# Performance work log

Measured on AMD Instinct MI355X. Metric: run time of the kernel, lower is better.

## Reference

```python
import jax, jax.numpy as jnp
import numpy as np
from jax import lax

BN_EPS = 1e-5
ARC_EPS = 1e-7
M = 0.5   # margin
S = 64.0  # scale


def _conv_block(x, w, g, b, a, stride):
    # Conv2d(bias=False, VALID) + BatchNorm2d (training mode, batch stats) + PReLU
    y = lax.conv_general_dilated(x, w, (stride, stride), 'VALID',
                                 dimension_numbers=('NCHW', 'OIHW', 'NCHW'))
    mu = y.mean((0, 2, 3), keepdims=True)
    var = ((y - mu) ** 2).mean((0, 2, 3), keepdims=True)
    y = (y - mu) * lax.rsqrt(var + BN_EPS) * g.reshape(1, -1, 1, 1) + b.reshape(1, -1, 1, 1)
    return jnp.where(y > 0, y, a * y)


def setup_inputs() -> dict:
    key = jax.random.key(0)
    ks = jax.random.split(key, 16)
    N = 4096
    d = {}
    d['x'] = jax.random.normal(ks[0], (N, 1, 28, 28), jnp.float32)
    d['labels'] = jax.random.randint(ks[1], (N,), 0, 10)
    conv_shapes = [(32, 1, 1, 1), (64, 32, 3, 3), (32, 64, 1, 1),
                   (64, 32, 3, 3), (32, 64, 1, 1), (64, 32, 3, 3)]
    for i, s in enumerate(conv_shapes):
        fan_in = s[1] * s[2] * s[3]
        d[f'cw{i}'] = jax.random.normal(ks[2 + i], s, jnp.float32) / np.sqrt(fan_in)
        d[f'bg{i}'] = jnp.ones((s[0],), jnp.float32)
        d[f'bb{i}'] = jnp.zeros((s[0],), jnp.float32)
        d[f'pa{i}'] = jnp.full((), 0.25, jnp.float32)  # nn.PReLU() single param
    d['lw1'] = jax.random.normal(ks[8], (128, 1024), jnp.float32) * (1.0 / np.sqrt(1024))
    d['lg1'] = jnp.ones((128,), jnp.float32)
    d['lb1'] = jnp.zeros((128,), jnp.float32)
    d['pl1'] = jnp.full((), 0.25, jnp.float32)
    d['lw2'] = jax.random.normal(ks[9], (2, 128), jnp.float32) * (1.0 / np.sqrt(128))
    d['lb2'] = jnp.zeros((2,), jnp.float32)
    d['aw'] = jax.random.normal(ks[10], (10, 2), jnp.float32) * 0.2  # ArcLoss fc weight (out, in)
    return d


def reference(x, labels, cw0, cw1, cw2, cw3, cw4, cw5,
              bg0, bb0, bg1, bb1, bg2, bb2, bg3, bb3, bg4, bb4, bg5, bb5,
              pa0, pa1, pa2, pa3, pa4, pa5,
              lw1, lg1, lb1, pl1, lw2, lb2, aw):
    strides = (1, 2, 1, 2, 1, 1)
    ws = (cw0, cw1, cw2, cw3, cw4, cw5)
    gs = (bg0, bg1, bg2, bg3, bg4, bg5)
    bs = (bb0, bb1, bb2, bb3, bb4, bb5)
    pas = (pa0, pa1, pa2, pa3, pa4, pa5)
    h = x
    for w, g, b, a, st in zip(ws, gs, bs, pas, strides):
        h = _conv_block(h, w, g, b, a, st)  # final: (N, 64, 4, 4)
    flat = h.reshape(h.shape[0], -1)        # (N, 1024)
    z = flat @ lw1.T                         # (N, 128)
    mu = z.mean(0)
    var = ((z - mu) ** 2).mean(0)
    z = (z - mu) * lax.rsqrt(var + BN_EPS) * lg1 + lb1
    z = jnp.where(z > 0, z, pl1 * z)
    features = z @ lw2.T + lb2               # (N, 2)

    # ArcLoss. NOTE: original torch code's weight-normalization loop is a no-op
    # (rebinds local var), so fc weight is used UN-normalized; only x is normalized.
    xn = features / jnp.linalg.norm(features, axis=-1, keepdims=True)
    wf = xn @ aw.T                           # (N, 10) logits
    n = wf.shape[0]
    tgt = wf[jnp.arange(n), labels]          # vectorized diag gather
    num = S * jnp.cos(jnp.arccos(jnp.clip(tgt, -1.0 + ARC_EPS, 1.0 - ARC_EPS)) + M)
    # vectorized exclusion sum: sum_j exp(s*wf[i,j]) minus the target column
    den = jnp.exp(num) + jnp.sum(jnp.exp(S * wf), axis=1) - jnp.exp(S * tgt)
    loss = -jnp.mean(num - jnp.log(den))
    return (features, wf, loss)
```

## Files before the change

kernel.cpp:

```cpp
#include <hip/hip_runtime.h>
#include <hip/hip_bf16.h>
#include <math.h>


typedef __attribute__((ext_vector_type(8))) short s16x8;
typedef __attribute__((ext_vector_type(16))) float f32x16;

__device__ __forceinline__ unsigned short f2bf(float f) {
  __hip_bfloat16 h = __float2bfloat16(f);
  unsigned short u;
  __builtin_memcpy(&u, &h, 2);
  return u;
}
__device__ __forceinline__ float bf2f(unsigned short h) {
  union { unsigned int u; float f; } t; t.u = ((unsigned int)h) << 16; return t.f;
}

__global__ __launch_bounds__(256) void kRedX(const float* __restrict__ x,
                                             float* __restrict__ part) {
  int tid = threadIdx.x;
  int b = blockIdx.x;
  const float4* x4 = (const float4*)x;
  float s = 0.f, q = 0.f;
  for (size_t i = (size_t)b * 256 + tid; i < 802816; i += (size_t)512 * 256) {
    float4 v = x4[i];
    s += v.x + v.y + v.z + v.w;
    q += v.x * v.x + v.y * v.y + v.z * v.z + v.w * v.w;
  }
#pragma unroll
  for (int off = 32; off; off >>= 1) {
    s += __shfl_down(s, off);
    q += __shfl_down(q, off);
  }
  __shared__ float ls[4][2];
  int w = tid >> 6;
  if ((tid & 63) == 0) { ls[w][0] = s; ls[w][1] = q; }
  __syncthreads();
  if (tid == 0) {
    part[b * 2]     = ls[0][0] + ls[1][0] + ls[2][0] + ls[3][0];
    part[b * 2 + 1] = ls[0][1] + ls[1][1] + ls[2][1] + ls[3][1];
  }
}

__global__ __launch_bounds__(256) void kRedPart(const float* __restrict__ part,
                                                float* __restrict__ outp, int nb, int C2) {
  int slot = blockIdx.x;
  int tid = threadIdx.x;
  float s = 0.f;
  for (int i = tid; i < nb; i += 256) s += part[(size_t)i * C2 + slot];
#pragma unroll
  for (int off = 32; off; off >>= 1) s += __shfl_down(s, off);
  __shared__ float ls[4];
  if ((tid & 63) == 0) ls[tid >> 6] = s;
  __syncthreads();
  if (tid == 0) outp[slot] = ls[0] + ls[1] + ls[2] + ls[3];
}

__global__ __launch_bounds__(256) void kPrepW(const float* __restrict__ cw1,
                                              unsigned short* __restrict__ wf) {
  int tid = threadIdx.x;
  int lane = tid & 63, fb = tid >> 6;
  int m = lane & 31, kg = lane >> 5;
  for (int pass = 0; pass < 9; pass++) {
    int f = pass * 4 + fb;
    int tap = f >> 2, rem = f & 3, kt = rem >> 1, nt = rem & 1;
    int o = nt * 32 + m;
    int kb = kt * 16 + kg * 8;
    union { s16x8 v; unsigned short e[8]; } u;
#pragma unroll
    for (int j = 0; j < 8; j++)
      u.e[j] = f2bf(cw1[(size_t)o * 288 + (size_t)(kb + j) * 9 + tap]);
    ((s16x8*)wf)[f * 64 + lane] = u.v;
  }
}

__global__ __launch_bounds__(256) void kPrepW3(const float* __restrict__ cw3,
                                               unsigned short* __restrict__ wf3) {
  int tid = threadIdx.x;
  int lane = tid & 63, fq = tid >> 6;
  int m = lane & 31, kg = lane >> 5;
  for (int pass = 0; pass < 9; pass++) {
    int f = pass * 4 + fq;
    int s = f >> 1, nt = f & 1;
    int tap = s >> 1;
    int o = nt * 32 + m;
    int c0 = (s & 1) * 16 + kg * 8;
    union { s16x8 v; unsigned short e[8]; } u;
#pragma unroll
    for (int j = 0; j < 8; j++)
      u.e[j] = f2bf(cw3[(size_t)o * 288 + (size_t)(c0 + j) * 9 + tap]);
    ((s16x8*)wf3)[f * 64 + lane] = u.v;
  }
}

__global__ __launch_bounds__(256) void kPrepW1x1(const float* __restrict__ wgt,
                                                 unsigned short* __restrict__ wfb) {
  int tid = threadIdx.x;
  int l = tid & 63, ks = tid >> 6;
  int o = l & 31, kg = l >> 5;
  union { s16x8 v; unsigned short e[8]; } u;
#pragma unroll
  for (int j = 0; j < 8; j++) {
    int c = ks * 16 + kg * 8 + j;
    u.e[j] = f2bf(wgt[o * 64 + c]);
  }
  ((s16x8*)wfb)[ks * 64 + l] = u.v;
}

__global__ __launch_bounds__(256, 2) void kConv1(
    const float* __restrict__ x, const float* __restrict__ cw0,
    const float* __restrict__ bg0, const float* __restrict__ bb0,
    const float* __restrict__ pa0, const unsigned short* __restrict__ wf,
    const float* __restrict__ sx, unsigned short* __restrict__ y1b,
    float* __restrict__ part) {
  __shared__ __align__(16) unsigned short h0t[25088];
  __shared__ __align__(16) float xbuf[784];
  __shared__ float s0[32], t0[32];
  int tid = threadIdx.x;
  int n = blockIdx.x;
  int l = tid & 63, w = tid >> 6;
  int nt = w & 1, mh = w >> 1;
  int m = l & 31, kg = l >> 5;

  s16x8 bfr[9][2];
  const s16x8* wfp = (const s16x8*)wf;
#pragma unroll
  for (int tap = 0; tap < 9; tap++)
#pragma unroll
    for (int kt = 0; kt < 2; kt++)
      bfr[tap][kt] = wfp[(tap * 4 + kt * 2 + nt) * 64 + l];

  if (tid < 196) ((float4*)xbuf)[tid] = ((const float4*)(x + (size_t)n * 784))[tid];
  if (tid < 32) {
    const float invM = 1.0f / (4096.0f * 784.0f);
    float mux = sx[0] * invM;
    float varx = fmaxf(sx[1] * invM - mux * mux, 0.0f);
    float w0 = cw0[tid];
    float inv = rsqrtf(w0 * w0 * varx + 1e-5f);
    float sc = w0 * bg0[tid] * inv;
    s0[tid] = sc;
    t0[tid] = bb0[tid] - mux * sc;
  }
  __syncthreads();

  float a0p = *pa0;
  int g = tid & 3;
  float sg[8], tg[8];
#pragma unroll
  for (int j = 0; j < 8; j++) { sg[j] = s0[g * 8 + j]; tg[j] = t0[g * 8 + j]; }
  char* h0b = (char*)h0t;
  int koffW = g * 16;
  for (int t = 0; t < 13; t++) {
    int p = (tid >> 2) + t * 64;
    if (p < 784) {
      float xv = xbuf[p];
      union { s16x8 v; unsigned short e[8]; } u;
#pragma unroll
      for (int j = 0; j < 8; j++) {
        float v = fmaf(xv, sg[j], tg[j]);
        v = v > 0.f ? v : a0p * v;
        u.e[j] = f2bf(v);
      }
      int ad = ((p << 6) + koffW) ^ (((p >> 1) & 7) << 4);
      *(s16x8*)(h0b + ad) = u.v;
    }
  }
  __syncthreads();

  int pixb[3];
#pragma unroll
  for (int mt = 0; mt < 3; mt++) {
    int p = (mh * 3 + mt) * 32 + m;
    p = p > 168 ? 168 : p;
    pixb[mt] = (p / 13) * 56 + (p % 13) * 2;
  }
  int koffA = kg * 16;

#define Z16 {0.f,0.f,0.f,0.f, 0.f,0.f,0.f,0.f, 0.f,0.f,0.f,0.f, 0.f,0.f,0.f,0.f}
  f32x16 acc0 = Z16, acc1 = Z16, acc2 = Z16;

#define MT_STEP(ACC, MTL) { int pb = pixb[MTL]; \
  _Pragma("unroll") for (int tap = 0; tap < 9; tap++) { \
    int pix = pb + (tap / 3) * 28 + (tap % 3); \
    int ad = ((pix << 6) + koffA) ^ (((pix >> 1) & 7) << 4); \
    s16x8 a0 = *(const s16x8*)(h0b + ad); \
    s16x8 a1 = *(const s16x8*)(h0b + (ad ^ 32)); \
    ACC = __builtin_amdgcn_mfma_f32_32x32x16_bf16(a0, bfr[tap][0], ACC, 0, 0, 0); \
    ACC = __builtin_amdgcn_mfma_f32_32x32x16_bf16(a1, bfr[tap][1], ACC, 0, 0, 0); \
  } }

  MT_STEP(acc0, 0)
  MT_STEP(acc1, 1)
  MT_STEP(acc2, 2)
#undef MT_STEP

  __syncthreads();
  unsigned short* ystage = h0t;
  float* sSf = xbuf;
  float* sQf = xbuf + 128;
  float s = 0.f, q = 0.f;
  int och = nt * 32 + m;
#define ST_MT(ACC, MTL) { int pbase = (mh * 3 + MTL) * 32 + (kg << 2); \
  _Pragma("unroll") for (int r = 0; r < 16; r++) { \
    int p = pbase + (r & 3) + ((r >> 2) << 3); \
    if (p < 169) { float v = ACC[r]; \
      ystage[p * 64 + och] = f2bf(v); s += v; q += v * v; } } }

  ST_MT(acc0, 0)
  ST_MT(acc1, 1)
  ST_MT(acc2, 2)
#undef ST_MT

  s += __shfl_xor(s, 32);
  q += __shfl_xor(q, 32);
  if (l < 32) { sSf[w * 32 + l] = s; sQf[w * 32 + l] = q; }
  __syncthreads();
  {
    const s16x8* src8 = (const s16x8*)ystage;
    s16x8* dst8 = (s16x8*)(y1b + (size_t)n * 10816);
    for (int e = tid; e < 1352; e += 256) dst8[e] = src8[e];
  }
  if (tid < 64) {
    int o = tid, wv = o >> 5;
    part[(size_t)n * 128 + o] = sSf[wv * 32 + (o & 31)] + sSf[(wv + 2) * 32 + (o & 31)];
  } else if (tid < 128) {
    int o = tid - 64, wv = o >> 5;
    part[(size_t)n * 128 + 64 + o] = sQf[wv * 32 + (o & 31)] + sQf[(wv + 2) * 32 + (o & 31)];
  }
}

__global__ __launch_bounds__(256, 4) void kConv1x1m(
    const unsigned short* __restrict__ wfb, const float* __restrict__ g,
    const float* __restrict__ b, const float* __restrict__ pa,
    const float* __restrict__ stats, float invM,
    const unsigned short* __restrict__ in, unsigned short* __restrict__ outb,
    float* __restrict__ part) {
  __shared__ __align__(16) unsigned short hs[128 * 64];
  __shared__ float scs[64], shs[64];
  __shared__ float sS[4][32], sQ[4][32];
  int tid = threadIdx.x;
  size_t r0 = (size_t)blockIdx.x * 128;
  int l = tid & 63, w = tid >> 6;
  int m = l & 31, kg = l >> 5;

  s16x8 bfr[4];
  const s16x8* bp = (const s16x8*)wfb;
#pragma unroll
  for (int ks = 0; ks < 4; ks++) bfr[ks] = bp[ks * 64 + l];

  if (tid < 64) {
    float mu = stats[tid] * invM;
    float va = fmaxf(stats[64 + tid] * invM - mu * mu, 0.0f);
    float iv = rsqrtf(va + 1e-5f);
    float sc = g[tid] * iv;
    scs[tid] = sc;
    shs[tid] = b[tid] - mu * sc;
  }
  __syncthreads();
  float al = *pa;
  char* hb = (char*)hs;
#pragma unroll
  for (int i = 0; i < 4; i++) {
    int e = tid + i * 256;
    int row = e >> 3, seg = e & 7;
    union { s16x8 v; unsigned short e8[8]; } u, o8;
    u.v = *(const s16x8*)(in + (r0 + row) * 64 + seg * 8);
#pragma unroll
    for (int j = 0; j < 8; j++) {
      int c = seg * 8 + j;
      float h = fmaf(bf2f(u.e8[j]), scs[c], shs[c]);
      h = h > 0.f ? h : al * h;
      o8.e8[j] = f2bf(h);
    }
    int ad = (row * 128 + seg * 16) ^ ((row & 7) << 4);
    *(s16x8*)(hb + ad) = o8.v;
  }
  __syncthreads();

#define Z16 {0.f,0.f,0.f,0.f, 0.f,0.f,0.f,0.f, 0.f,0.f,0.f,0.f, 0.f,0.f,0.f,0.f}
  f32x16 acc = Z16;
#undef Z16
  int rloc = w * 32 + m;
  int abase = (rloc * 128 + kg * 16) ^ ((rloc & 7) << 4);
#pragma unroll
  for (int ks = 0; ks < 4; ks++) {
    s16x8 a = *(const s16x8*)(hb + (abase ^ (ks * 32)));
    acc = __builtin_amdgcn_mfma_f32_32x32x16_bf16(a, bfr[ks], acc, 0, 0, 0);
  }

  float ss = 0.f, qq = 0.f;
#pragma unroll
  for (int rr = 0; rr < 16; rr++) {
    int rowt = (rr & 3) + ((rr >> 2) << 3) + (kg << 2);
    float v = acc[rr];
    outb[(r0 + (size_t)w * 32 + rowt) * 32 + m] = f2bf(v);
    ss += v; qq += v * v;
  }
  ss += __shfl_xor(ss, 32);
  qq += __shfl_xor(qq, 32);
  if (l < 32) { sS[w][l] = ss; sQ[w][l] = qq; }
  __syncthreads();
  if (tid < 32) {
    part[(size_t)blockIdx.x * 64 + tid] = sS[0][tid] + sS[1][tid] + sS[2][tid] + sS[3][tid];
  } else if (tid < 64) {
    int o = tid - 32;
    part[(size_t)blockIdx.x * 64 + 32 + o] = sQ[0][o] + sQ[1][o] + sQ[2][o] + sQ[3][o];
  }
}

__global__ __launch_bounds__(256, 3) void kConv3m(
    const unsigned short* __restrict__ wf3, const float* __restrict__ g,
    const float* __restrict__ b, const float* __restrict__ pa,
    const float* __restrict__ stats, const unsigned short* __restrict__ in,
    unsigned short* __restrict__ outb, float* __restrict__ part) {
  __shared__ __align__(16) unsigned short h2t[169 * 32];
  __shared__ float scs[32], shs[32];
  __shared__ float sS[4][32], sQ[4][32];
  int tid = threadIdx.x;
  int n = blockIdx.x;
  int l = tid & 63, w = tid >> 6;
  int nt = w & 1, mt = w >> 1;
  int m = l & 31, kg = l >> 5;

  s16x8 bfr[18];
  const s16x8* wfp = (const s16x8*)wf3;
#pragma unroll
  for (int s = 0; s < 18; s++) bfr[s] = wfp[(s * 2 + nt) * 64 + l];

  if (tid < 32) {
    const float invM = 1.0f / 692224.0f;
    float mu = stats[tid] * invM;
    float va = fmaxf(stats[32 + tid] * invM - mu * mu, 0.0f);
    float iv = rsqrtf(va + 1e-5f);
    float sc = g[tid] * iv;
    scs[tid] = sc;
    shs[tid] = b[tid] - mu * sc;
  }
  __syncthreads();
  float al = *pa;
  char* hb = (char*)h2t;
  for (int e = tid; e < 676; e += 256) {
    int p = e >> 2, q = e & 3;
    union { s16x8 v; unsigned short e8[8]; } u, o8;
    u.v = ((const s16x8*)(in + ((size_t)n * 169 + p) * 32))[q];
#pragma unroll
    for (int j = 0; j < 8; j++) {
      int c = q * 8 + j;
      float h = fmaf(bf2f(u.e8[j]), scs[c], shs[c]);
      h = h > 0.f ? h : al * h;
      o8.e8[j] = f2bf(h);
    }
    int ad = ((p << 6) + q * 16) ^ (((p >> 1) & 7) << 4);
    *(s16x8*)(hb + ad) = o8.v;
  }
  __syncthreads();

  int p = mt * 32 + m;
  p = p > 35 ? 35 : p;
  int pixb = (p / 6) * 26 + (p % 6) * 2;

#define Z16 {0.f,0.f,0.f,0.f, 0.f,0.f,0.f,0.f, 0.f,0.f,0.f,0.f, 0.f,0.f,0.f,0.f}
  f32x16 acc = Z16;
#undef Z16
#pragma unroll
  for (int s = 0; s < 18; s++) {
    int tap = s >> 1;
    int pix = pixb + (tap / 3) * 13 + (tap % 3);
    int ad = ((pix << 6) + (s & 1) * 32 + kg * 16) ^ (((pix >> 1) & 7) << 4);
    s16x8 a = *(const s16x8*)(hb + ad);
    acc = __builtin_amdgcn_mfma_f32_32x32x16_bf16(a, bfr[s], acc, 0, 0, 0);
  }

  float ss = 0.f, qq = 0.f;
  int och = nt * 32 + m;
#pragma unroll
  for (int r = 0; r < 16; r++) {
    int row = (r & 3) + ((r >> 2) << 3) + (kg << 2);
    int pp = mt * 32 + row;
    if (pp < 36) {
      float v = acc[r];
      outb[((size_t)n * 36 + pp) * 64 + och] = f2bf(v);
      ss += v; qq += v * v;
    }
  }
  ss += __shfl_xor(ss, 32);
  qq += __shfl_xor(qq, 32);
  if (l < 32) { sS[w][l] = ss; sQ[w][l] = qq; }
  __syncthreads();
  if (tid < 64) {
    int o = tid, wv = o >> 5;
    part[(size_t)n * 128 + o] = sS[wv][o & 31] + sS[wv + 2][o & 31];
  } else if (tid < 128) {
    int o = tid - 64, wv = o >> 5;
    part[(size_t)n * 128 + 64 + o] = sQ[wv][o & 31] + sQ[wv + 2][o & 31];
  }
}

__global__ __launch_bounds__(128) void kConv5m(
    const unsigned short* __restrict__ wf5, const float* __restrict__ g,
    const float* __restrict__ b, const float* __restrict__ pa,
    const float* __restrict__ stats, const unsigned short* __restrict__ in,
    float* __restrict__ outb, float* __restrict__ part) {
  __shared__ __align__(16) unsigned short h4t[2 * 1280];
  __shared__ float scs[32], shs[32];
  int tid = threadIdx.x;
  int nA = blockIdx.x * 2;
  int l = tid & 63, w = tid >> 6;
  int m = l & 31, kg = l >> 5;

  s16x8 bfr[18];
  const s16x8* wfp = (const s16x8*)wf5;
#pragma unroll
  for (int s = 0; s < 18; s++) bfr[s] = wfp[(s * 2 + w) * 64 + l];

  if (tid < 32) {
    const float invM = 1.0f / 147456.0f;
    float mu = stats[tid] * invM;
    float va = fmaxf(stats[32 + tid] * invM - mu * mu, 0.0f);
    float iv = rsqrtf(va + 1e-5f);
    float sc = g[tid] * iv;
    scs[tid] = sc;
    shs[tid] = b[tid] - mu * sc;
  }
  __syncthreads();
  float al = *pa;
  char* hb = (char*)h4t;
  for (int e = tid; e < 288; e += 128) {
    int img = e >= 144;
    int rem = e - img * 144;
    int p = rem >> 2, q = rem & 3;
    union { s16x8 v; unsigned short e8[8]; } u, o8;
    u.v = ((const s16x8*)(in + ((size_t)(nA + img) * 36 + p) * 32))[q];
#pragma unroll
    for (int j = 0; j < 8; j++) {
      int c = q * 8 + j;
      float h = fmaf(bf2f(u.e8[j]), scs[c], shs[c]);
      h = h > 0.f ? h : al * h;
      o8.e8[j] = f2bf(h);
    }
    int ad = img * 2560 + (((p << 6) + q * 16) ^ (((p >> 1) & 7) << 4));
    *(s16x8*)(hb + ad) = o8.v;
  }
  __syncthreads();

  int imgl = m >> 4;
  int pl = m & 15;
  int pixb = (pl >> 2) * 6 + (pl & 3);
  int ibase = imgl * 2560;

#define Z16 {0.f,0.f,0.f,0.f, 0.f,0.f,0.f,0.f, 0.f,0.f,0.f,0.f, 0.f,0.f,0.f,0.f}
  f32x16 acc = Z16;
#undef Z16
#pragma unroll
  for (int s = 0; s < 18; s++) {
    int tap = s >> 1;
    int pix = pixb + (tap / 3) * 6 + (tap % 3);
    int ad = ibase + (((pix << 6) + (s & 1) * 32 + kg * 16) ^ (((pix >> 1) & 7) << 4));
    s16x8 a = *(const s16x8*)(hb + ad);
    acc = __builtin_amdgcn_mfma_f32_32x32x16_bf16(a, bfr[s], acc, 0, 0, 0);
  }

  float ss = 0.f, qq = 0.f;
  int och = w * 32 + m;
#pragma unroll
  for (int r = 0; r < 16; r++) {
    int row = (r & 3) + ((r >> 2) << 3) + (kg << 2);
    int img = row >> 4, p = row & 15;
    float v = acc[r];
    outb[(size_t)(nA + img) * 1024 + och * 16 + p] = v;
    ss += v; qq += v * v;
  }
  ss += __shfl_xor(ss, 32);
  qq += __shfl_xor(qq, 32);
  if (l < 32) {
    part[(size_t)blockIdx.x * 128 + w * 32 + l] = ss;
    part[(size_t)blockIdx.x * 128 + 64 + w * 32 + l] = qq;
  }
}

__global__ __launch_bounds__(256) void kPrepLW(const float* __restrict__ lw1,
                                               unsigned short* __restrict__ wfl) {
  int tid = threadIdx.x;
  int lane = tid & 63, fq = tid >> 6;
  int m = lane & 31, kg = lane >> 5;
  for (int pp = 0; pp < 4; pp++) {
    int f_idx = (blockIdx.x * 4 + pp) * 4 + fq;
    int ks = f_idx >> 2, nt = f_idx & 3;
    int f = nt * 32 + m;
    int kb = ks * 16 + kg * 8;
    const float4* src = (const float4*)(lw1 + (size_t)f * 1024 + kb);
    float4 v0 = src[0], v1 = src[1];
    float t[8] = {v0.x, v0.y, v0.z, v0.w, v1.x, v1.y, v1.z, v1.w};
    union { s16x8 v; unsigned short e[8]; } u;
#pragma unroll
    for (int j = 0; j < 8; j++) u.e[j] = f2bf(t[j]);
    ((s16x8*)wfl)[f_idx * 64 + lane] = u.v;
  }
}

__global__ __launch_bounds__(128) void kFC1m(
    const unsigned short* __restrict__ wfl, const float* __restrict__ g,
    const float* __restrict__ b, const float* __restrict__ pa,
    const float* __restrict__ stats, const float* __restrict__ y5,
    float* __restrict__ z, float* __restrict__ part) {
  __shared__ __align__(16) unsigned short hs[32 * 1024];
  __shared__ float scs[64], shs[64];
  int tid = threadIdx.x;
  int n0 = blockIdx.x * 32;
  if (tid < 64) {
    const float invM = 1.0f / 65536.0f;
    float mu = stats[tid] * invM;
    float va = fmaxf(stats[64 + tid] * invM - mu * mu, 0.0f);
    float iv = rsqrtf(va + 1e-5f);
    float sc = g[tid] * iv;
    scs[tid] = sc;
    shs[tid] = b[tid] - mu * sc;
  }
  __syncthreads();
  float al = *pa;
  char* hb = (char*)hs;
  for (int i = 0; i < 32; i++) {
    int sgi = tid + i * 128;
    int nn = sgi >> 7, k8 = sgi & 127;
    int c = k8 >> 1;
    float sc = scs[c], sh = shs[c];
    const float4* src = (const float4*)(y5 + (size_t)(n0 + nn) * 1024 + k8 * 8);
    float4 v0 = src[0], v1 = src[1];
    float t[8] = {v0.x, v0.y, v0.z, v0.w, v1.x, v1.y, v1.z, v1.w};
    union { s16x8 v; unsigned short e[8]; } u;
#pragma unroll
    for (int j = 0; j < 8; j++) {
      float h = fmaf(t[j], sc, sh);
      h = h > 0.f ? h : al * h;
      u.e[j] = f2bf(h);
    }
    int ad = (nn * 2048 + k8 * 16) ^ ((nn & 7) << 4);
    *(s16x8*)(hb + ad) = u.v;
  }
  __syncthreads();

  int l = tid & 63, w = tid >> 6;
  int m = l & 31, kg = l >> 5;
#define Z16 {0.f,0.f,0.f,0.f, 0.f,0.f,0.f,0.f, 0.f,0.f,0.f,0.f, 0.f,0.f,0.f,0.f}
  f32x16 acc0 = Z16, acc1 = Z16;
#undef Z16
  const s16x8* bp = (const s16x8*)wfl;
  int abase = (m * 2048 + kg * 16) ^ ((m & 7) << 4);
#pragma unroll 4
  for (int ks = 0; ks < 64; ks++) {
    s16x8 a = *(const s16x8*)(hb + (abase ^ (ks * 32)));
    s16x8 b0 = bp[(ks * 4 + 2 * w + 0) * 64 + l];
    s16x8 b1 = bp[(ks * 4 + 2 * w + 1) * 64 + l];
    acc0 = __builtin_amdgcn_mfma_f32_32x32x16_bf16(a, b0, acc0, 0, 0, 0);
    acc1 = __builtin_amdgcn_mfma_f32_32x32x16_bf16(a, b1, acc1, 0, 0, 0);
  }

  float s0 = 0.f, q0 = 0.f, s1 = 0.f, q1 = 0.f;
  int f0c = (2 * w) * 32 + m, f1c = (2 * w + 1) * 32 + m;
#pragma unroll
  for (int r = 0; r < 16; r++) {
    int n = (r & 3) + ((r >> 2) << 3) + (kg << 2);
    float v0 = acc0[r], v1 = acc1[r];
    z[(size_t)(n0 + n) * 128 + f0c] = v0;
    z[(size_t)(n0 + n) * 128 + f1c] = v1;
    s0 += v0; q0 += v0 * v0; s1 += v1; q1 += v1 * v1;
  }
  s0 += __shfl_xor(s0, 32); q0 += __shfl_xor(q0, 32);
  s1 += __shfl_xor(s1, 32); q1 += __shfl_xor(q1, 32);
  if (l < 32) {
    size_t base = (size_t)blockIdx.x * 256;
    part[base + w * 64 + m] = s0;
    part[base + w * 64 + 32 + m] = s1;
    part[base + 128 + w * 64 + m] = q0;
    part[base + 128 + w * 64 + 32 + m] = q1;
  }
}

__global__ __launch_bounds__(256) void kFC2Arc(
    const float* __restrict__ z, const float* __restrict__ s6,
    const float* __restrict__ lg1, const float* __restrict__ lb1,
    const float* __restrict__ pl1, const float* __restrict__ lw2,
    const float* __restrict__ lb2, const float* __restrict__ aw,
    const int* __restrict__ labels, float* __restrict__ out,
    float* __restrict__ lpart) {
  __shared__ float scz[128], shz[128], w2a[128], w2b[128];
  __shared__ float awl[20];
  __shared__ float lred[4];
  int tid = threadIdx.x;
  if (tid < 128) {
    const float invM = 1.0f / 4096.0f;
    float mu = s6[tid] * invM;
    float va = fmaxf(s6[128 + tid] * invM - mu * mu, 0.0f);
    float iv = rsqrtf(va + 1e-5f);
    float sc = lg1[tid] * iv;
    scz[tid] = sc;
    shz[tid] = lb1[tid] - mu * sc;
    w2a[tid] = lw2[tid];
    w2b[tid] = lw2[128 + tid];
  }
  if (tid < 20) awl[tid] = aw[tid];
  __syncthreads();
  float al = *pl1;
  int n = blockIdx.x * 256 + tid;
  const float4* zr = (const float4*)(z + (size_t)n * 128);
  float f0 = lb2[0], f1 = lb2[1];
#pragma unroll
  for (int kb = 0; kb < 32; kb++) {
    float4 v = zr[kb];
    float hv[4] = {v.x, v.y, v.z, v.w};
#pragma unroll
    for (int u = 0; u < 4; u++) {
      int k = kb * 4 + u;
      float h = fmaf(hv[u], scz[k], shz[k]);
      h = h > 0.f ? h : al * h;
      f0 = fmaf(h, w2a[k], f0);
      f1 = fmaf(h, w2b[k], f1);
    }
  }
  out[(size_t)n * 2] = f0;
  out[(size_t)n * 2 + 1] = f1;
  float nrm = sqrtf(fmaxf(f0 * f0 + f1 * f1, 1e-30f));
  float xn0 = f0 / nrm, xn1 = f1 / nrm;
  int lab = labels[n];
  float wv[10];
  float m64 = -3.4e38f;
#pragma unroll
  for (int j = 0; j < 10; j++) {
    float w = xn0 * awl[2 * j] + xn1 * awl[2 * j + 1];
    wv[j] = w;
    out[8192 + (size_t)n * 10 + j] = w;
    m64 = fmaxf(m64, 64.0f * w);
  }
  float tgt = wv[0];
#pragma unroll
  for (int j = 1; j < 10; j++) if (j == lab) tgt = wv[j];
  if (lab == 0) tgt = wv[0];
  const float CLO = (float)(-1.0 + 1e-7);
  const float CHI = (float)(1.0 - 1e-7);
  float t = fminf(fmaxf(tgt, CLO), CHI);
  float num = 64.0f * (t * 0.87758256189037276f - 0.47942553860420301f * sqrtf(fmaxf(1.0f - t * t, 0.0f)));
  float L = fmaxf(num, m64);
  float dsum = expf(num - L) - expf(64.0f * tgt - L);
#pragma unroll
  for (int j = 0; j < 10; j++) dsum += expf(64.0f * wv[j] - L);
  dsum = fmaxf(dsum, 1e-30f);
  float li = num - (L + logf(dsum));
#pragma unroll
  for (int off = 32; off; off >>= 1) li += __shfl_down(li, off);
  if ((tid & 63) == 0) lred[tid >> 6] = li;
  __syncthreads();
  if (tid == 0) lpart[blockIdx.x] = lred[0] + lred[1] + lred[2] + lred[3];
}

__global__ void kFinal(const float* __restrict__ lpart, float* __restrict__ out) {
  int tid = threadIdx.x;
  float v = (tid < 16) ? lpart[tid] : 0.f;
#pragma unroll
  for (int off = 8; off; off >>= 1) v += __shfl_down(v, off);
  if (tid == 0) out[49152] = -v * (1.0f / 4096.0f);
}

extern "C" void kernel_launch(void* const* d_in, const int* in_sizes, int n_in,
                              void* d_out, int out_size, void* d_ws, size_t ws_size,
                              hipStream_t stream) {
  const float* x   = (const float*)d_in[0];
  const int* labels = (const int*)d_in[1];
  const float* cw0 = (const float*)d_in[2];
  const float* bg0 = (const float*)d_in[3];
  const float* bb0 = (const float*)d_in[4];
  const float* pa0 = (const float*)d_in[5];
  const float* cw1 = (const float*)d_in[6];
  const float* bg1 = (const float*)d_in[7];
  const float* bb1 = (const float*)d_in[8];
  const float* pa1 = (const float*)d_in[9];
  const float* cw2 = (const float*)d_in[10];
  const float* bg2 = (const float*)d_in[11];
  const float* bb2 = (const float*)d_in[12];
  const float* pa2 = (const float*)d_in[13];
  const float* cw3 = (const float*)d_in[14];
  const float* bg3 = (const float*)d_in[15];
  const float* bb3 = (const float*)d_in[16];
  const float* pa3 = (const float*)d_in[17];
  const float* cw4 = (const float*)d_in[18];
  const float* bg4 = (const float*)d_in[19];
  const float* bb4 = (const float*)d_in[20];
  const float* pa4 = (const float*)d_in[21];
  const float* cw5 = (const float*)d_in[22];
  const float* bg5 = (const float*)d_in[23];
  const float* bb5 = (const float*)d_in[24];
  const float* pa5 = (const float*)d_in[25];
  const float* lw1 = (const float*)d_in[26];
  const float* lg1 = (const float*)d_in[27];
  const float* lb1 = (const float*)d_in[28];
  const float* pl1 = (const float*)d_in[29];
  const float* lw2 = (const float*)d_in[30];
  const float* lb2 = (const float*)d_in[31];
  const float* aw  = (const float*)d_in[32];
  float* out = (float*)d_out;
  float* ws = (float*)d_ws;

  float* PX = ws;
  float* SX = ws + 1024;
  float* S1 = ws + 1040;
  float* S2 = ws + 1168;
  float* S3 = ws + 1232;
  float* S4 = ws + 1360;
  float* S5 = ws + 1424;
  float* S6 = ws + 1552;
  float* LP = ws + 1808;
  float* P1 = ws + 2048;
  float* P2 = P1 + 524288;
  float* P3 = P2 + 346112;
  float* P4 = P3 + 524288;
  float* P5 = P4 + 73728;
  float* P6 = P1;
  unsigned short* Y1 = (unsigned short*)(ws + (size_t)2097152);
  unsigned short* Y2 = Y1 + (size_t)44302336;
  unsigned short* Y3 = Y2 + (size_t)22151168;
  unsigned short* Y4 = Y3 + (size_t)9437184;
  float* Y5 = (float*)(Y4 + (size_t)4718592);
  float* Z  = Y5 + (size_t)4194304;
  float* WF = Z + 524288;
  float* WFL = WF + 16384;
  float* WF3 = WFL + 65536;
  float* WC2 = WF3 + 16384;
  float* WC4 = WC2 + 1024;
  float* WF5 = WC4 + 1024;

  kPrepW<<<1, 256, 0, stream>>>(cw1, (unsigned short*)WF);
  kPrepW3<<<1, 256, 0, stream>>>(cw3, (unsigned short*)WF3);
  kPrepW3<<<1, 256, 0, stream>>>(cw5, (unsigned short*)WF5);
  kPrepW1x1<<<1, 256, 0, stream>>>(cw2, (unsigned short*)WC2);
  kPrepW1x1<<<1, 256, 0, stream>>>(cw4, (unsigned short*)WC4);
  kPrepLW<<<16, 256, 0, stream>>>(lw1, (unsigned short*)WFL);
  kRedX<<<512, 256, 0, stream>>>(x, PX);
  kRedPart<<<2, 256, 0, stream>>>(PX, SX, 512, 2);
  kConv1<<<4096, 256, 0, stream>>>(x, cw0, bg0, bb0, pa0, (const unsigned short*)WF, SX, Y1, P1);
  kRedPart<<<128, 256, 0, stream>>>(P1, S1, 4096, 128);
  kConv1x1m<<<5408, 256, 0, stream>>>((const unsigned short*)WC2, bg1, bb1, pa1, S1,
                                      1.0f / 692224.0f, Y1, Y2, P2);
  kRedPart<<<64, 256, 0, stream>>>(P2, S2, 5408, 64);
  kConv3m<<<4096, 256, 0, stream>>>((const unsigned short*)WF3, bg2, bb2, pa2, S2, Y2, Y3, P3);
  kRedPart<<<128, 256, 0, stream>>>(P3, S3, 4096, 128);
  kConv1x1m<<<1152, 256, 0, stream>>>((const unsigned short*)WC4, bg3, bb3, pa3, S3,
                                      1.0f / 147456.0f, Y3, Y4, P4);
  kRedPart<<<64, 256, 0, stream>>>(P4, S4, 1152, 64);
  kConv5m<<<2048, 128, 0, stream>>>((const unsigned short*)WF5, bg4, bb4, pa4, S4, Y4, Y5, P5);
  kRedPart<<<128, 256, 0, stream>>>(P5, S5, 2048, 128);
  kFC1m<<<128, 128, 0, stream>>>((const unsigned short*)WFL, bg5, bb5, pa5, S5, Y5, Z, P6);
  kRedPart<<<256, 256, 0, stream>>>(P6, S6, 128, 256);
  kFC2Arc<<<16, 256, 0, stream>>>(Z, S6, lg1, lb1, pl1, lw2, lb2, aw, labels, out, LP);
  kFinal<<<1, 64, 0, stream>>>(LP, out);
}
```

Baseline: 242.3 us.

## Split conv1 per-image work across two blocks by output rows

The first 3x3 stride-2 conv kernel now launches two blocks per image, each computing half the output rows (91 or 78 positions) from the matching slice of input rows. This halves LDS use per block (smaller activation tile and input buffer), which can allow more resident blocks, and doubles the grid for better load balance. In exchange, the overlapping input rows are recomputed, the wave work is uneven (one wave pair does two tiles, the other one), and the partial-stats buffer doubles, so workspace offsets and the reduction count change.

Result: no change. 237.7 us (-1.9%).

```diff
diff --git a/kernel.cpp b/kernel.cpp
--- a/kernel.cpp
+++ b/kernel.cpp
@@ -113,14 +113,17 @@
     const float* __restrict__ pa0, const unsigned short* __restrict__ wf,
     const float* __restrict__ sx, unsigned short* __restrict__ y1b,
     float* __restrict__ part) {
-  __shared__ __align__(16) unsigned short h0t[25088];
-  __shared__ __align__(16) float xbuf[784];
+  __shared__ __align__(16) unsigned short h0t[13440];
+  __shared__ __align__(16) float xbuf[420];
   __shared__ float s0[32], t0[32];
   int tid = threadIdx.x;
-  int n = blockIdx.x;
+  int n = blockIdx.x >> 1, half = blockIdx.x & 1;
   int l = tid & 63, w = tid >> 6;
-  int nt = w & 1, mh = w >> 1;
+  int nt = w & 1, mpair = w >> 1;
   int m = l & 31, kg = l >> 5;
+  int npos = half ? 78 : 91;
+  int xoff = half ? 392 : 0;
+  int nxpix = half ? 364 : 420;
 
   s16x8 bfr[9][2];
   const s16x8* wfp = (const s16x8*)wf;
@@ -130,7 +133,11 @@
     for (int kt = 0; kt < 2; kt++)
       bfr[tap][kt] = wfp[(tap * 4 + kt * 2 + nt) * 64 + l];
 
-  if (tid < 196) ((float4*)xbuf)[tid] = ((const float4*)(x + (size_t)n * 784))[tid];
+  {
+    int nx4 = half ? 91 : 105;
+    if (tid < nx4)
+      ((float4*)xbuf)[tid] = ((const float4*)(x + (size_t)n * 784 + xoff))[tid];
+  }
   if (tid < 32) {
     const float invM = 1.0f / (4096.0f * 784.0f);
     float mux = sx[0] * invM;
@@ -150,9 +157,9 @@
   for (int j = 0; j < 8; j++) { sg[j] = s0[g * 8 + j]; tg[j] = t0[g * 8 + j]; }
   char* h0b = (char*)h0t;
   int koffW = g * 16;
-  for (int t = 0; t < 13; t++) {
+  for (int t = 0; t < 7; t++) {
     int p = (tid >> 2) + t * 64;
-    if (p < 784) {
+    if (p < nxpix) {
       float xv = xbuf[p];
       union { s16x8 v; unsigned short e[8]; } u;
 #pragma unroll
@@ -167,21 +174,19 @@
   }
   __syncthreads();
 
-  int pixb[3];
-#pragma unroll
-  for (int mt = 0; mt < 3; mt++) {
-    int p = (mh * 3 + mt) * 32 + m;
-    p = p > 168 ? 168 : p;
-    pixb[mt] = (p / 13) * 56 + (p % 13) * 2;
-  }
+  int tA = mpair ? 2 : 0;
+  int lpA = tA * 32 + m; lpA = lpA > npos - 1 ? npos - 1 : lpA;
+  int lpB = 32 + m;      lpB = lpB > npos - 1 ? npos - 1 : lpB;
+  int pixbA = (lpA / 13) * 56 + (lpA % 13) * 2;
+  int pixbB = (lpB / 13) * 56 + (lpB % 13) * 2;
   int koffA = kg * 16;
 
 #define Z16 {0.f,0.f,0.f,0.f, 0.f,0.f,0.f,0.f, 0.f,0.f,0.f,0.f, 0.f,0.f,0.f,0.f}
-  f32x16 acc0 = Z16, acc1 = Z16, acc2 = Z16;
-
-#define MT_STEP(ACC, MTL) { int pb = pixb[MTL]; \
+  f32x16 acc0 = Z16, acc1 = Z16;
+
+#define MT_STEP(ACC, PB) { \
   _Pragma("unroll") for (int tap = 0; tap < 9; tap++) { \
-    int pix = pb + (tap / 3) * 28 + (tap % 3); \
+    int pix = (PB) + (tap / 3) * 28 + (tap % 3); \
     int ad = ((pix << 6) + koffA) ^ (((pix >> 1) & 7) << 4); \
     s16x8 a0 = *(const s16x8*)(h0b + ad); \
     s16x8 a1 = *(const s16x8*)(h0b + (ad ^ 32)); \
@@ -189,9 +194,8 @@
     ACC = __builtin_amdgcn_mfma_f32_32x32x16_bf16(a1, bfr[tap][1], ACC, 0, 0, 0); \
   } }
 
-  MT_STEP(acc0, 0)
-  MT_STEP(acc1, 1)
-  MT_STEP(acc2, 2)
+  MT_STEP(acc0, pixbA)
+  if (mpair == 0) { MT_STEP(acc1, pixbB) }
 #undef MT_STEP
 
   __syncthreads();
@@ -200,15 +204,14 @@
   float* sQf = xbuf + 128;
   float s = 0.f, q = 0.f;
   int och = nt * 32 + m;
-#define ST_MT(ACC, MTL) { int pbase = (mh * 3 + MTL) * 32 + (kg << 2); \
+#define ST_MT(ACC, TILE) { int pbase = (TILE) * 32 + (kg << 2); \
   _Pragma("unroll") for (int r = 0; r < 16; r++) { \
     int p = pbase + (r & 3) + ((r >> 2) << 3); \
-    if (p < 169) { float v = ACC[r]; \
+    if (p < npos) { float v = ACC[r]; \
       ystage[p * 64 + och] = f2bf(v); s += v; q += v * v; } } }
 
-  ST_MT(acc0, 0)
-  ST_MT(acc1, 1)
-  ST_MT(acc2, 2)
+  ST_MT(acc0, tA)
+  if (mpair == 0) { ST_MT(acc1, 1) }
 #undef ST_MT
 
   s += __shfl_xor(s, 32);
@@ -216,16 +219,19 @@
   if (l < 32) { sSf[w * 32 + l] = s; sQf[w * 32 + l] = q; }
   __syncthreads();
   {
+    int nseg = npos * 8;
     const s16x8* src8 = (const s16x8*)ystage;
-    s16x8* dst8 = (s16x8*)(y1b + (size_t)n * 10816);
-    for (int e = tid; e < 1352; e += 256) dst8[e] = src8[e];
+    s16x8* dst8 = (s16x8*)(y1b + (size_t)n * 10816 + half * 5824);
+    for (int e = tid; e < nseg; e += 256) dst8[e] = src8[e];
   }
   if (tid < 64) {
     int o = tid, wv = o >> 5;
-    part[(size_t)n * 128 + o] = sSf[wv * 32 + (o & 31)] + sSf[(wv + 2) * 32 + (o & 31)];
+    part[(size_t)blockIdx.x * 128 + o] =
+        sSf[wv * 32 + (o & 31)] + sSf[(wv + 2) * 32 + (o & 31)];
   } else if (tid < 128) {
     int o = tid - 64, wv = o >> 5;
-    part[(size_t)n * 128 + 64 + o] = sQf[wv * 32 + (o & 31)] + sQf[(wv + 2) * 32 + (o & 31)];
+    part[(size_t)blockIdx.x * 128 + 64 + o] =
+        sQf[wv * 32 + (o & 31)] + sQf[(wv + 2) * 32 + (o & 31)];
   }
 }
 
@@ -709,12 +715,12 @@
   float* S6 = ws + 1552;
   float* LP = ws + 1808;
   float* P1 = ws + 2048;
-  float* P2 = P1 + 524288;
+  float* P2 = P1 + 1048576;
   float* P3 = P2 + 346112;
   float* P4 = P3 + 524288;
   float* P5 = P4 + 73728;
   float* P6 = P1;
-  unsigned short* Y1 = (unsigned short*)(ws + (size_t)2097152);
+  unsigned short* Y1 = (unsigned short*)(ws + (size_t)2359296);
   unsigned short* Y2 = Y1 + (size_t)44302336;
   unsigned short* Y3 = Y2 + (size_t)22151168;
   unsigned short* Y4 = Y3 + (size_t)9437184;
@@ -735,8 +741,8 @@
   kPrepLW<<<16, 256, 0, stream>>>(lw1, (unsigned short*)WFL);
   kRedX<<<512, 256, 0, stream>>>(x, PX);
   kRedPart<<<2, 256, 0, stream>>>(PX, SX, 512, 2);
-  kConv1<<<4096, 256, 0, stream>>>(x, cw0, bg0, bb0, pa0, (const unsigned short*)WF, SX, Y1, P1);
-  kRedPart<<<128, 256, 0, stream>>>(P1, S1, 4096, 128);
+  kConv1<<<8192, 256, 0, stream>>>(x, cw0, bg0, bb0, pa0, (const unsigned short*)WF, SX, Y1, P1);
+  kRedPart<<<128, 256, 0, stream>>>(P1, S1, 8192, 128);
   kConv1x1m<<<5408, 256, 0, stream>>>((const unsigned short*)WC2, bg1, bb1, pa1, S1,
                                       1.0f / 692224.0f, Y1, Y2, P2);
   kRedPart<<<64, 256, 0, stream>>>(P2, S2, 5408, 64);
```
